# Kernel optimization log

Measured on AMD Instinct MI355X. Metric: run time of the kernel, lower is better.

The kernel has to match this reference:

```python
import jax, jax.numpy as jnp
import numpy as np

HOURS = 24
ALPHA, BETA, GAMMA, DELTA = 1.0, 2.0, 1.0, 0.5
TEMP = 0.1
WIN = 2  # window_size in _peak_shape_loss
NEG = -1e9

B, S = 16384, 1440  # 60 days of hourly data


def setup_inputs() -> dict:
    key = jax.random.key(0)
    k1, k2 = jax.random.split(key)
    y_pred = jax.random.normal(k1, (B, S), dtype=jnp.float32)
    y_true = jax.random.normal(k2, (B, S), dtype=jnp.float32)
    # default daytime mask from the module: hour in [6, 20]
    hours = jnp.tile(jnp.arange(HOURS), S // HOURS)  # (S,)
    day = ((hours >= 6) & (hours <= 20)).astype(jnp.float32)
    is_daytime = jnp.broadcast_to(day, (B, S))
    return {"y_pred": y_pred, "y_true": y_true, "is_daytime": is_daytime}


def _soft_peaks(y, day_mask):
    # y, day_mask: (B, D, H) -> soft peak values/times per day: (B, D)
    masked = jnp.where(day_mask > 0.5, y, NEG)
    attn = jax.nn.softmax(masked / TEMP, axis=-1)
    vals = jnp.sum(attn * y, axis=-1)
    t = jnp.arange(HOURS, dtype=y.dtype)
    times = jnp.sum(attn * t, axis=-1)
    return vals, times


def reference(y_pred, y_true, is_daytime):
    b, s = y_true.shape
    d = s // HOURS
    yp = y_pred[:, : d * HOURS].reshape(b, d, HOURS)
    yt = y_true[:, : d * HOURS].reshape(b, d, HOURS)
    dm = is_daytime[:, : d * HOURS].reshape(b, d, HOURS)

    L_overall = jnp.mean((y_pred - y_true) ** 2)

    tv, tt = _soft_peaks(yt, dm)
    pv, pt = _soft_peaks(yp, dm)
    L_mag = jnp.mean((pv - tv) ** 2)
    L_time = jnp.mean((pt - tt) ** 2)

    masked_true = jnp.where(dm > 0.5, yt, NEG)
    peak = jnp.argmax(masked_true, axis=-1)  # (B, D) int
    offs = jnp.arange(-WIN, WIN + 1)
    idx = peak[..., None] + offs  # (B, D, 5)
    valid = (idx >= 0) & (idx < HOURS)  # emulates window clipping at day edges
    idx_c = jnp.clip(idx, 0, HOURS - 1)
    tw = jnp.take_along_axis(yt, idx_c, axis=-1)  # (B, D, 5)
    pw = jnp.take_along_axis(yp, idx_c, axis=-1)
    vmask = valid.astype(yt.dtype)
    cnt = jnp.sum(vmask, axis=-1)  # window length per (B, D)
    tmax = jnp.max(jnp.where(valid, tw, -jnp.inf), axis=-1, keepdims=True)
    pmax = jnp.max(jnp.where(valid, pw, -jnp.inf), axis=-1, keepdims=True)
    tn = tw / (tmax + 1e-6)
    pn = pw / (pmax + 1e-6)
    per = jnp.sum((pn - tn) ** 2 * vmask, axis=-1) / cnt  # per-window MSE
    L_shape = jnp.sum(per) / (b * d + 1e-6)

    return ALPHA * L_overall + BETA * L_mag + GAMMA * L_time + DELTA * L_shape
```

## Files before the change

kernel.cpp:

```cpp
#include <hip/hip_runtime.h>
#include <math.h>


#define HOURS_ 24
#define WIN_ 2
#define NEGV (-1e9f)

__device__ __forceinline__ float frcp(float x) { return __builtin_amdgcn_rcpf(x); }

#define DPP_XOR1 0xB1
#define DPP_XOR2 0x4E

template<int CTRL>
__device__ __forceinline__ int dpp_i(int src) {
    return __builtin_amdgcn_update_dpp(0, src, CTRL, 0xF, 0xF, true);
}
template<int CTRL>
__device__ __forceinline__ float dpp_f(float x) {
    return __int_as_float(dpp_i<CTRL>(__float_as_int(x)));
}

__device__ __forceinline__ void seg_body(
    float2 p0, float2 p1, float2 p2,
    float2 t0, float2 t1, float2 t2,
    float2 m0, float2 m1, float2 m2,
    int seg, float vfl,
    float& o, float& mg, float& tl, float& sh)
{
    const int h0 = seg * 6;
    float a[6]  = {p0.x, p0.y, p1.x, p1.y, p2.x, p2.y};
    float b[6]  = {t0.x, t0.y, t1.x, t1.y, t2.x, t2.y};
    float dm[6] = {m0.x, m0.y, m1.x, m1.y, m2.x, m2.y};

    float oo = 0.f;
    #pragma unroll
    for (int k = 0; k < 6; ++k) { float d = a[k] - b[k]; oo = fmaf(d, d, oo); }
    o = fmaf(oo, vfl, o);

    float bm[6], am[6];
    #pragma unroll
    for (int k = 0; k < 6; ++k) {
        bool dy = dm[k] > 0.5f;
        bm[k] = dy ? b[k] : NEGV;
        am[k] = dy ? a[k] : NEGV;
    }

    bool  s0 = bm[1] > bm[0]; float v01 = s0 ? bm[1] : bm[0]; int i01 = s0 ? h0+1 : h0;
    bool  s1 = bm[3] > bm[2]; float v23 = s1 ? bm[3] : bm[2]; int i23 = s1 ? h0+3 : h0+2;
    bool  s2 = bm[5] > bm[4]; float v45 = s2 ? bm[5] : bm[4]; int i45 = s2 ? h0+5 : h0+4;
    bool  tA = v23 > v01; float mt = tA ? v23 : v01; int pk = tA ? i23 : i01;
    bool  tB = v45 > mt;  mt = tB ? v45 : mt;        pk = tB ? i45 : pk;
    float mp = fmaxf(fmaxf(fmaxf(am[0], am[1]), fmaxf(am[2], am[3])),
                     fmaxf(am[4], am[5]));

    {
        float mt_o = dpp_f<DPP_XOR1>(mt); int pk_o = dpp_i<DPP_XOR1>(pk);
        float mp_o = dpp_f<DPP_XOR1>(mp);
        bool to = (mt_o > mt) || (mt_o == mt && pk_o < pk);
        pk = to ? pk_o : pk; mt = fmaxf(mt, mt_o); mp = fmaxf(mp, mp_o);
        mt_o = dpp_f<DPP_XOR2>(mt); pk_o = dpp_i<DPP_XOR2>(pk);
        mp_o = dpp_f<DPP_XOR2>(mp);
        to = (mt_o > mt) || (mt_o == mt && pk_o < pk);
        pk = to ? pk_o : pk; mt = fmaxf(mt, mt_o); mp = fmaxf(mp, mp_o);
    }

    float mt10 = mt * 10.f, mp10 = mp * 10.f;
    float set = 0.f, syt = 0.f, sht = 0.f;
    float sep = 0.f, syp = 0.f, shp = 0.f;
    #pragma unroll
    for (int k = 0; k < 6; ++k) {
        float et = __expf(fmaf(bm[k], 10.f, -mt10));
        float ep = __expf(fmaf(am[k], 10.f, -mp10));
        float hh = (float)(h0 + k);
        set += et; syt = fmaf(et, b[k], syt); sht = fmaf(et, hh, sht);
        sep += ep; syp = fmaf(ep, a[k], syp); shp = fmaf(ep, hh, shp);
    }
    set += dpp_f<DPP_XOR1>(set); set += dpp_f<DPP_XOR2>(set);
    syt += dpp_f<DPP_XOR1>(syt); syt += dpp_f<DPP_XOR2>(syt);
    sht += dpp_f<DPP_XOR1>(sht); sht += dpp_f<DPP_XOR2>(sht);
    sep += dpp_f<DPP_XOR1>(sep); sep += dpp_f<DPP_XOR2>(sep);
    syp += dpp_f<DPP_XOR1>(syp); syp += dpp_f<DPP_XOR2>(syp);
    shp += dpp_f<DPP_XOR1>(shp); shp += dpp_f<DPP_XOR2>(shp);
    {
        float rs = frcp(set), rq = frcp(sep);
        float d1 = syp * rq - syt * rs;
        float d2 = shp * rq - sht * rs;
        float once = (seg == 0) ? vfl : 0.f;
        mg = fmaf(d1 * d1, once, mg);
        tl = fmaf(d2 * d2, once, tl);
    }

    int lo = pk - WIN_; lo = lo < 0 ? 0 : lo;
    int hi = pk + WIN_; hi = hi > 23 ? 23 : hi;
    int cnt = hi - lo + 1;
    float invcnt = (cnt == 5) ? 0.2f : ((cnt == 4) ? 0.25f : (1.f / 3.f));
    float twm = -INFINITY, pwm = -INFINITY;
    #pragma unroll
    for (int k = 0; k < 6; ++k) {
        int hg = h0 + k;
        bool in = (hg >= lo) && (hg <= hi);
        twm = in ? fmaxf(twm, b[k]) : twm;
        pwm = in ? fmaxf(pwm, a[k]) : pwm;
    }
    twm = fmaxf(twm, dpp_f<DPP_XOR1>(twm)); twm = fmaxf(twm, dpp_f<DPP_XOR2>(twm));
    pwm = fmaxf(pwm, dpp_f<DPP_XOR1>(pwm)); pwm = fmaxf(pwm, dpp_f<DPP_XOR2>(pwm));
    {
        float rt = frcp(twm + 1e-6f);
        float rp = frcp(pwm + 1e-6f);
        float ss = 0.f;
        #pragma unroll
        for (int k = 0; k < 6; ++k) {
            int hg = h0 + k;
            bool in = (hg >= lo) && (hg <= hi);
            float d = fmaf(a[k], rp, -(b[k] * rt));
            ss = in ? fmaf(d, d, ss) : ss;
        }
        sh = fmaf(ss * invcnt, vfl, sh);
    }
}

__global__ __launch_bounds__(256) void splloss_days(
    const float* __restrict__ ypred,
    const float* __restrict__ ytrue,
    const float* __restrict__ isday,
    float4* __restrict__ partials,
    int n_days, int nit)
{
    const int tid = threadIdx.x;
    const int seg = tid & 3;
    const int grp = tid >> 2;
    const int dayStride = gridDim.x * 64;
    const int segOff = seg * 6;

    int day = blockIdx.x * 64 + grp;

    float o = 0.f, mg = 0.f, tl = 0.f, sh = 0.f;

    int   dA = day < n_days ? day : 0;
    float vA = day < n_days ? 1.f : 0.f;
    {
        const float2* p = reinterpret_cast<const float2*>(ypred + (size_t)dA * 24 + segOff);
        const float2* t = reinterpret_cast<const float2*>(ytrue + (size_t)dA * 24 + segOff);
        const float2* m = reinterpret_cast<const float2*>(isday + (size_t)dA * 24 + segOff);
        float2 a0 = p[0], a1 = p[1], a2 = p[2];
        float2 b0 = t[0], b1 = t[1], b2 = t[2];
        float2 c0 = m[0], c1 = m[1], c2 = m[2];

        for (int it = 0; it < nit; ++it) {
            int   dayN = day + dayStride;
            int   dB = dayN < n_days ? dayN : 0;
            float vB = dayN < n_days ? 1.f : 0.f;
            const float2* pN = reinterpret_cast<const float2*>(ypred + (size_t)dB * 24 + segOff);
            const float2* tN = reinterpret_cast<const float2*>(ytrue + (size_t)dB * 24 + segOff);
            const float2* mN = reinterpret_cast<const float2*>(isday + (size_t)dB * 24 + segOff);
            float2 e0 = pN[0], e1 = pN[1], e2 = pN[2];
            float2 f0 = tN[0], f1 = tN[1], f2 = tN[2];
            float2 g0 = mN[0], g1 = mN[1], g2 = mN[2];
            __builtin_amdgcn_sched_barrier(0);

            seg_body(a0, a1, a2, b0, b1, b2, c0, c1, c2, seg, vA, o, mg, tl, sh);

            a0 = e0; a1 = e1; a2 = e2;
            b0 = f0; b1 = f1; b2 = f2;
            c0 = g0; c1 = g1; c2 = g2;
            vA = vB; day = dayN;
        }
    }

    #pragma unroll
    for (int off = 32; off > 0; off >>= 1) {
        o  += __shfl_down(o,  off);
        mg += __shfl_down(mg, off);
        tl += __shfl_down(tl, off);
        sh += __shfl_down(sh, off);
    }
    __shared__ float4 red[4];
    int wid = threadIdx.x >> 6;
    if ((threadIdx.x & 63) == 0) red[wid] = make_float4(o, mg, tl, sh);
    __syncthreads();
    if (threadIdx.x == 0) {
        float4 r0 = red[0], r1 = red[1], r2 = red[2], r3 = red[3];
        partials[blockIdx.x] = make_float4(r0.x + r1.x + r2.x + r3.x,
                                           r0.y + r1.y + r2.y + r3.y,
                                           r0.z + r1.z + r2.z + r3.z,
                                           r0.w + r1.w + r2.w + r3.w);
    }
}

__global__ __launch_bounds__(256) void splloss_final(
    const float4* __restrict__ partials, int nb, float* __restrict__ out,
    double inv_bs, double inv_bd, double inv_shape)
{
    double o = 0.0, m = 0.0, t = 0.0, s = 0.0;
    for (int i = threadIdx.x; i < nb; i += 256) {
        float4 p = partials[i];
        o += (double)p.x; m += (double)p.y; t += (double)p.z; s += (double)p.w;
    }
    #pragma unroll
    for (int off = 32; off > 0; off >>= 1) {
        o += __shfl_down(o, off);
        m += __shfl_down(m, off);
        t += __shfl_down(t, off);
        s += __shfl_down(s, off);
    }
    __shared__ double red[4][4];
    int wid = threadIdx.x >> 6;
    if ((threadIdx.x & 63) == 0) { red[wid][0] = o; red[wid][1] = m; red[wid][2] = t; red[wid][3] = s; }
    __syncthreads();
    if (threadIdx.x == 0) {
        double ot = red[0][0] + red[1][0] + red[2][0] + red[3][0];
        double mt = red[0][1] + red[1][1] + red[2][1] + red[3][1];
        double tt = red[0][2] + red[1][2] + red[2][2] + red[3][2];
        double st = red[0][3] + red[1][3] + red[2][3] + red[3][3];
        double total = 1.0 * (ot * inv_bs)
                     + 2.0 * (mt * inv_bd)
                     + 1.0 * (tt * inv_bd)
                     + 0.5 * (st * inv_shape);
        out[0] = (float)total;
    }
}

extern "C" void kernel_launch(void* const* d_in, const int* in_sizes, int n_in,
                              void* d_out, int out_size, void* d_ws, size_t ws_size,
                              hipStream_t stream) {
    const float* yp = (const float*)d_in[0];
    const float* yt = (const float*)d_in[1];
    const float* dm = (const float*)d_in[2];
    float* out = (float*)d_out;

    int n = in_sizes[0];
    int n_days = n / HOURS_;

    int nb = (n_days + 63) / 64;
    if (nb > 1536) nb = 1536;
    int perIter = nb * 64;
    int nit = (n_days + perIter - 1) / perIter;

    float4* partials = (float4*)d_ws;

    splloss_days<<<nb, 256, 0, stream>>>(yp, yt, dm, partials, n_days, nit);

    double inv_bs    = 1.0 / (double)n;
    double inv_bd    = 1.0 / (double)n_days;
    double inv_shape = 1.0 / ((double)n_days + 1e-6);
    splloss_final<<<1, 256, 0, stream>>>(partials, nb, out, inv_bs, inv_bd, inv_shape);
}
```

Measured before the change: 272.6 us.

## Stage day tiles through LDS with coalesced float4 loads

Replaces the per-thread strided float2 register loads and their register double-buffered prefetch with a cooperative tile load. Each block copies 64 days of all three arrays into shared memory using contiguous float4 reads, then each thread reads its 6-hour segment from LDS. The goal is fully coalesced global reads. In exchange it adds two block barriers per tile, LDS traffic and possible bank conflicts, and it drops the software prefetch that overlapped loads with compute.

```diff
diff --git a/kernel.cpp b/kernel.cpp
--- a/kernel.cpp
+++ b/kernel.cpp
@@ -5,6 +5,10 @@
 #define HOURS_ 24
 #define WIN_ 2
 #define NEGV (-1e9f)
+#define DPB 64
+#define DSTR 28
+#define CH_PER_ARR (DPB * 6)
+#define CH_TOTAL (CH_PER_ARR * 3)
 
 __device__ __forceinline__ float frcp(float x) { return __builtin_amdgcn_rcpf(x); }
 
@@ -20,17 +24,16 @@
     return __int_as_float(dpp_i<CTRL>(__float_as_int(x)));
 }
 
-__device__ __forceinline__ void seg_body(
-    float2 p0, float2 p1, float2 p2,
-    float2 t0, float2 t1, float2 t2,
-    float2 m0, float2 m1, float2 m2,
+__device__ __forceinline__ void seg_body_lds(
+    const float* __restrict__ ap, const float* __restrict__ bp,
+    const float* __restrict__ mp,
     int seg, float vfl,
     float& o, float& mg, float& tl, float& sh)
 {
     const int h0 = seg * 6;
-    float a[6]  = {p0.x, p0.y, p1.x, p1.y, p2.x, p2.y};
-    float b[6]  = {t0.x, t0.y, t1.x, t1.y, t2.x, t2.y};
-    float dm[6] = {m0.x, m0.y, m1.x, m1.y, m2.x, m2.y};
+    float a[6], b[6], dm[6];
+    #pragma unroll
+    for (int k = 0; k < 6; ++k) { a[k] = ap[h0 + k]; b[k] = bp[h0 + k]; dm[k] = mp[h0 + k]; }
 
     float oo = 0.f;
     #pragma unroll
@@ -50,21 +53,21 @@
     bool  s2 = bm[5] > bm[4]; float v45 = s2 ? bm[5] : bm[4]; int i45 = s2 ? h0+5 : h0+4;
     bool  tA = v23 > v01; float mt = tA ? v23 : v01; int pk = tA ? i23 : i01;
     bool  tB = v45 > mt;  mt = tB ? v45 : mt;        pk = tB ? i45 : pk;
-    float mp = fmaxf(fmaxf(fmaxf(am[0], am[1]), fmaxf(am[2], am[3])),
-                     fmaxf(am[4], am[5]));
+    float mp2 = fmaxf(fmaxf(fmaxf(am[0], am[1]), fmaxf(am[2], am[3])),
+                      fmaxf(am[4], am[5]));
 
     {
         float mt_o = dpp_f<DPP_XOR1>(mt); int pk_o = dpp_i<DPP_XOR1>(pk);
-        float mp_o = dpp_f<DPP_XOR1>(mp);
+        float mp_o = dpp_f<DPP_XOR1>(mp2);
         bool to = (mt_o > mt) || (mt_o == mt && pk_o < pk);
-        pk = to ? pk_o : pk; mt = fmaxf(mt, mt_o); mp = fmaxf(mp, mp_o);
+        pk = to ? pk_o : pk; mt = fmaxf(mt, mt_o); mp2 = fmaxf(mp2, mp_o);
         mt_o = dpp_f<DPP_XOR2>(mt); pk_o = dpp_i<DPP_XOR2>(pk);
-        mp_o = dpp_f<DPP_XOR2>(mp);
+        mp_o = dpp_f<DPP_XOR2>(mp2);
         to = (mt_o > mt) || (mt_o == mt && pk_o < pk);
-        pk = to ? pk_o : pk; mt = fmaxf(mt, mt_o); mp = fmaxf(mp, mp_o);
-    }
-
-    float mt10 = mt * 10.f, mp10 = mp * 10.f;
+        pk = to ? pk_o : pk; mt = fmaxf(mt, mt_o); mp2 = fmaxf(mp2, mp_o);
+    }
+
+    float mt10 = mt * 10.f, mp10 = mp2 * 10.f;
     float set = 0.f, syt = 0.f, sht = 0.f;
     float sep = 0.f, syp = 0.f, shp = 0.f;
     #pragma unroll
@@ -124,47 +127,42 @@
     const float* __restrict__ ytrue,
     const float* __restrict__ isday,
     float4* __restrict__ partials,
-    int n_days, int nit)
+    int n_days, int ntiles)
 {
-    const int tid = threadIdx.x;
-    const int seg = tid & 3;
-    const int grp = tid >> 2;
-    const int dayStride = gridDim.x * 64;
-    const int segOff = seg * 6;
-
-    int day = blockIdx.x * 64 + grp;
+    __shared__ float lds[3][DPB][DSTR];
+
+    const int tid   = threadIdx.x;
+    const int seg   = tid & 3;
+    const int dslot = tid >> 2;
 
     float o = 0.f, mg = 0.f, tl = 0.f, sh = 0.f;
 
-    int   dA = day < n_days ? day : 0;
-    float vA = day < n_days ? 1.f : 0.f;
-    {
-        const float2* p = reinterpret_cast<const float2*>(ypred + (size_t)dA * 24 + segOff);
-        const float2* t = reinterpret_cast<const float2*>(ytrue + (size_t)dA * 24 + segOff);
-        const float2* m = reinterpret_cast<const float2*>(isday + (size_t)dA * 24 + segOff);
-        float2 a0 = p[0], a1 = p[1], a2 = p[2];
-        float2 b0 = t[0], b1 = t[1], b2 = t[2];
-        float2 c0 = m[0], c1 = m[1], c2 = m[2];
-
-        for (int it = 0; it < nit; ++it) {
-            int   dayN = day + dayStride;
-            int   dB = dayN < n_days ? dayN : 0;
-            float vB = dayN < n_days ? 1.f : 0.f;
-            const float2* pN = reinterpret_cast<const float2*>(ypred + (size_t)dB * 24 + segOff);
-            const float2* tN = reinterpret_cast<const float2*>(ytrue + (size_t)dB * 24 + segOff);
-            const float2* mN = reinterpret_cast<const float2*>(isday + (size_t)dB * 24 + segOff);
-            float2 e0 = pN[0], e1 = pN[1], e2 = pN[2];
-            float2 f0 = tN[0], f1 = tN[1], f2 = tN[2];
-            float2 g0 = mN[0], g1 = mN[1], g2 = mN[2];
-            __builtin_amdgcn_sched_barrier(0);
-
-            seg_body(a0, a1, a2, b0, b1, b2, c0, c1, c2, seg, vA, o, mg, tl, sh);
-
-            a0 = e0; a1 = e1; a2 = e2;
-            b0 = f0; b1 = f1; b2 = f2;
-            c0 = g0; c1 = g1; c2 = g2;
-            vA = vB; day = dayN;
+    for (int t = blockIdx.x; t < ntiles; t += gridDim.x) {
+        const size_t baseDay = (size_t)t * DPB;
+
+        #pragma unroll
+        for (int j = 0; j < 5; ++j) {
+            int c = tid + j * 256;
+            if (c < CH_TOTAL) {
+                int arr = c / CH_PER_ARR;
+                int rem = c - arr * CH_PER_ARR;
+                int day = rem / 6;
+                int h0  = (rem - day * 6) * 4;
+                const float* g = (arr == 0) ? ypred : (arr == 1) ? ytrue : isday;
+                size_t gd = baseDay + (size_t)day;
+                float4 v = make_float4(0.f, 0.f, 0.f, 0.f);
+                if (gd < (size_t)n_days)
+                    v = *reinterpret_cast<const float4*>(g + gd * 24 + h0);
+                *reinterpret_cast<float4*>(&lds[arr][day][h0]) = v;
+            }
         }
+        __syncthreads();
+
+        size_t gday = baseDay + (size_t)dslot;
+        float vfl = gday < (size_t)n_days ? 1.f : 0.f;
+        seg_body_lds(&lds[0][dslot][0], &lds[1][dslot][0], &lds[2][dslot][0],
+                     seg, vfl, o, mg, tl, sh);
+        __syncthreads();
     }
 
     #pragma unroll
@@ -230,15 +228,13 @@
 
     int n = in_sizes[0];
     int n_days = n / HOURS_;
-
-    int nb = (n_days + 63) / 64;
-    if (nb > 1536) nb = 1536;
-    int perIter = nb * 64;
-    int nit = (n_days + perIter - 1) / perIter;
+    int ntiles = (n_days + DPB - 1) / DPB;
+
+    int nb = ntiles < 1536 ? ntiles : 1536;
 
     float4* partials = (float4*)d_ws;
 
-    splloss_days<<<nb, 256, 0, stream>>>(yp, yt, dm, partials, n_days, nit);
+    splloss_days<<<nb, 256, 0, stream>>>(yp, yt, dm, partials, n_days, ntiles);
 
     double inv_bs    = 1.0 / (double)n;
     double inv_bd    = 1.0 / (double)n_days;
```

New measurement: 285.0 us. +4.6%, slower.
